# Optimization experiments

Hardware: AMD Instinct MI355X
Metric: run time of the kernel (lower is better)

## Reference

```python
import jax, jax.numpy as jnp
import numpy as np

GROUP_SIZE = 128

def _dequantize(qweight, wscales, wzeros):
    # qweight: [N, K//2] packed bytes, two uint4 values per byte
    # low nibble = even k index, high nibble = odd k index
    N, Kh = qweight.shape
    K = Kh * 2
    low = qweight & 0xF
    high = (qweight >> 4) & 0xF
    w_int = jnp.stack([low, high], axis=-1).reshape(N, K).astype(jnp.float32)  # [N, K]
    G = K // GROUP_SIZE  # number of groups along K
    w_grp = w_int.reshape(N, G, GROUP_SIZE)
    s = wscales.T.reshape(N, G, 1)   # wscales: [G, N] -> [N, G, 1]
    z = wzeros.T.reshape(N, G, 1)
    return ((w_grp - z) * s).reshape(N, K)  # [N, K] dequantized

def setup_inputs() -> dict:
    key = jax.random.key(0)
    k1, k2, k3, k4, k5 = jax.random.split(key, 5)
    M, K, N = 4096, 4096, 12288
    G = K // GROUP_SIZE
    x = jax.random.normal(k1, (M, K), dtype=jnp.float32)
    qweight = jax.random.randint(k2, (N, K // 2), 0, 256, dtype=jnp.int32)
    wscales = jax.random.uniform(k3, (G, N), dtype=jnp.float32) * 0.05
    wzeros = jax.random.uniform(k4, (G, N), dtype=jnp.float32) * 15.0
    bias = jax.random.normal(k5, (N,), dtype=jnp.float32)
    return {"x": x, "qweight": qweight, "wscales": wscales, "wzeros": wzeros, "bias": bias}

def reference(x, qweight, wscales, wzeros, bias):
    # AWQ W4A16 linear: y = x @ dequant(W)^T + b
    w = _dequantize(qweight, wscales, wzeros)  # [N, K]
    return jnp.einsum('mk,nk->mn', x, w) + bias
```

## Files before the change

kernel.cpp:

```cpp
#include <hip/hip_runtime.h>

#define M_DIM 4096
#define K_DIM 4096
#define N_DIM 12288
#define BM 256
#define BN 256
#define BK 64
#define NT (K_DIM / BK)

typedef __bf16 bf16x8  __attribute__((ext_vector_type(8)));
typedef float  floatx16 __attribute__((ext_vector_type(16)));

__global__ __launch_bounds__(256) void xcast_kernel(const float* __restrict__ x,
                                                    __bf16* __restrict__ xb) {
    int idx = blockIdx.x * 256 + threadIdx.x;
    const float4* xv = (const float4*)x;
    float4 a = xv[idx * 2];
    float4 b = xv[idx * 2 + 1];
    bf16x8 o;
    o[0] = (__bf16)a.x; o[1] = (__bf16)a.y; o[2] = (__bf16)a.z; o[3] = (__bf16)a.w;
    o[4] = (__bf16)b.x; o[5] = (__bf16)b.y; o[6] = (__bf16)b.z; o[7] = (__bf16)b.w;
    ((bf16x8*)xb)[idx] = o;
}

__global__ __launch_bounds__(256) void dequant_kernel(const int* __restrict__ qw,
                                                      const float* __restrict__ scales,
                                                      const float* __restrict__ zeros,
                                                      __bf16* __restrict__ wb) {
    int idx = blockIdx.x * 256 + threadIdx.x;
    int n  = idx >> 9;
    int jq = (idx & 511) << 2;
    int g  = jq >> 6;
    float s = scales[g * N_DIM + n];
    float z = zeros[g * N_DIM + n];
    int4 q = *(const int4*)(qw + (size_t)n * (K_DIM / 2) + jq);
    bf16x8 o;
    o[0] = (__bf16)(((float)(q.x & 15)        - z) * s);
    o[1] = (__bf16)(((float)((q.x >> 4) & 15) - z) * s);
    o[2] = (__bf16)(((float)(q.y & 15)        - z) * s);
    o[3] = (__bf16)(((float)((q.y >> 4) & 15) - z) * s);
    o[4] = (__bf16)(((float)(q.z & 15)        - z) * s);
    o[5] = (__bf16)(((float)((q.z >> 4) & 15) - z) * s);
    o[6] = (__bf16)(((float)(q.w & 15)        - z) * s);
    o[7] = (__bf16)(((float)((q.w >> 4) & 15) - z) * s);
    *(bf16x8*)(wb + (size_t)n * K_DIM + (size_t)jq * 2) = o;
}

__global__ __launch_bounds__(512, 2) void gemm_kernel(const __bf16* __restrict__ A,
                                                      const __bf16* __restrict__ B,
                                                      const float* __restrict__ bias,
                                                      float* __restrict__ C) {
    __shared__ __bf16 As[2 * 2 * 256 * 32];
    __shared__ __bf16 Bs[2 * 2 * 256 * 32];

    const int tid  = threadIdx.x;
    const int wave = tid >> 6;
    const int lane = tid & 63;
    const int l32  = lane & 31;
    const int half = lane >> 5;
    const int side = wave >> 2;
    const int aw   = wave & 3;
    const int wm   = side * 128;
    const int wn   = aw * 64;
    const int bm0  = blockIdx.x * BM;
    const int bn0  = blockIdx.y * BN;

    const int r16  = lane >> 2;
    const int sl4  = lane & 3;
    const int bswz = ((lane >> 3) & 3) ^ ((lane >> 5) & 3);
    const int key0 = sl4 ^ bswz;
    const int key1 = key0 ^ 2;
    const __bf16* sA0 = A + (size_t)(bm0 + 32 * wave +      r16) * K_DIM + key0 * 8;
    const __bf16* sA1 = A + (size_t)(bm0 + 32 * wave + 16 + r16) * K_DIM + key1 * 8;
    const __bf16* sB0 = B + (size_t)(bn0 + 32 * wave +      r16) * K_DIM + key0 * 8;
    const __bf16* sB1 = B + (size_t)(bn0 + 32 * wave + 16 + r16) * K_DIM + key1 * 8;
    const int dst0 = wave * 1024;
    const int dst1 = wave * 1024 + 512;

    #define GLOAD(G, L) __builtin_amdgcn_global_load_lds( \
        (const __attribute__((address_space(1))) void*)(G), \
        (__attribute__((address_space(3))) void*)(L), 16, 0, 0)

    const int swzr = ((l32 >> 1) ^ (l32 >> 3)) & 3;
    const int koE  = ((half)     ^ swzr) << 3;
    const int koO  = ((2 | half) ^ swzr) << 3;
    const int rA0 = (wm +  0 + l32) * 32;
    const int rA1 = (wm + 32 + l32) * 32;
    const int rA2 = (wm + 64 + l32) * 32;
    const int rA3 = (wm + 96 + l32) * 32;
    const int rB0 = (wn +  0 + l32) * 32;
    const int rB1 = (wn + 32 + l32) * 32;

    #define MF(AF, BF, ACC) __builtin_amdgcn_mfma_f32_32x32x16_bf16((AF), (BF), (ACC), 0, 0, 0)

    floatx16 acc00 = {}, acc01 = {}, acc10 = {}, acc11 = {};
    floatx16 acc20 = {}, acc21 = {}, acc30 = {}, acc31 = {};

    GLOAD(sA0,      As + dst0);        GLOAD(sA1,      As + dst1);
    GLOAD(sB0,      Bs + dst0);        GLOAD(sB1,      Bs + dst1);
    GLOAD(sA0 + 32, As + 8192 + dst0); GLOAD(sA1 + 32, As + 8192 + dst1);
    GLOAD(sB0 + 32, Bs + 8192 + dst0); GLOAD(sB1 + 32, Bs + 8192 + dst1);
    asm volatile("s_waitcnt vmcnt(4)" ::: "memory");
    __builtin_amdgcn_s_barrier();

    #define READS(HOFF, KO) \
        a0 = *(const bf16x8*)(As + curo + (HOFF) + rA0 + (KO)); \
        b0 = *(const bf16x8*)(Bs + curo + (HOFF) + rB0 + (KO)); \
        a1 = *(const bf16x8*)(As + curo + (HOFF) + rA1 + (KO)); \
        b1 = *(const bf16x8*)(Bs + curo + (HOFF) + rB1 + (KO)); \
        a2 = *(const bf16x8*)(As + curo + (HOFF) + rA2 + (KO)); \
        a3 = *(const bf16x8*)(As + curo + (HOFF) + rA3 + (KO));

    #define MFMAS \
        __builtin_amdgcn_s_setprio(1); \
        acc00 = MF(a0, b0, acc00); acc10 = MF(a1, b0, acc10); \
        acc01 = MF(a0, b1, acc01); acc11 = MF(a1, b1, acc11); \
        acc20 = MF(a2, b0, acc20); acc21 = MF(a2, b1, acc21); \
        acc30 = MF(a3, b0, acc30); acc31 = MF(a3, b1, acc31); \
        __builtin_amdgcn_s_setprio(0);

    for (int kt = 0; kt < NT; ++kt) {
        const int curo = (kt & 1) * 16384;
        const int nxto = 16384 - curo;
        const int k0n  = ((kt + 1) & (NT - 1)) * BK;
        bf16x8 a0, a1, a2, a3, b0, b1;

        READS(0, koE);
        __builtin_amdgcn_s_barrier();
        MFMAS;
        __builtin_amdgcn_s_barrier();

        READS(0, koO);
        GLOAD(sA0 + k0n, As + nxto + dst0); GLOAD(sA1 + k0n, As + nxto + dst1);
        GLOAD(sB0 + k0n, Bs + nxto + dst0); GLOAD(sB1 + k0n, Bs + nxto + dst1);
        asm volatile("s_waitcnt vmcnt(4)" ::: "memory");
        __builtin_amdgcn_s_barrier();
        MFMAS;
        __builtin_amdgcn_s_barrier();

        READS(8192, koE);
        __builtin_amdgcn_s_barrier();
        MFMAS;
        __builtin_amdgcn_s_barrier();

        READS(8192, koO);
        GLOAD(sA0 + k0n + 32, As + nxto + 8192 + dst0);
        GLOAD(sA1 + k0n + 32, As + nxto + 8192 + dst1);
        GLOAD(sB0 + k0n + 32, Bs + nxto + 8192 + dst0);
        GLOAD(sB1 + k0n + 32, Bs + nxto + 8192 + dst1);
        asm volatile("s_waitcnt vmcnt(4)" ::: "memory");
        __builtin_amdgcn_s_barrier();
        MFMAS;
        __builtin_amdgcn_s_barrier();
    }

    #define EPI(ACC, MI, NI) { \
        const int col = bn0 + wn + (NI) * 32 + l32; \
        const float bv = bias[col]; \
        _Pragma("unroll") \
        for (int r = 0; r < 16; ++r) { \
            const int row = bm0 + wm + (MI) * 32 + half * 4 + (r & 3) + 8 * (r >> 2); \
            C[(size_t)row * N_DIM + col] = ACC[r] + bv; \
        } }
    EPI(acc00, 0, 0); EPI(acc01, 0, 1);
    EPI(acc10, 1, 0); EPI(acc11, 1, 1);
    EPI(acc20, 2, 0); EPI(acc21, 2, 1);
    EPI(acc30, 3, 0); EPI(acc31, 3, 1);
}

extern "C" void kernel_launch(void* const* d_in, const int* in_sizes, int n_in,
                              void* d_out, int out_size, void* d_ws, size_t ws_size,
                              hipStream_t stream) {
    const float* x      = (const float*)d_in[0];
    const int*   qw     = (const int*)d_in[1];
    const float* scales = (const float*)d_in[2];
    const float* zeros  = (const float*)d_in[3];
    const float* bias   = (const float*)d_in[4];
    float* out = (float*)d_out;

    __bf16* xb = (__bf16*)d_ws;
    __bf16* wb = (__bf16*)((char*)d_ws + (size_t)M_DIM * K_DIM * 2);

    xcast_kernel<<<(M_DIM * K_DIM / 8) / 256, 256, 0, stream>>>(x, xb);
    dequant_kernel<<<(N_DIM * (K_DIM / 2) / 4) / 256, 256, 0, stream>>>(qw, scales, zeros, wb);

    dim3 grid(M_DIM / BM, N_DIM / BN);
    gemm_kernel<<<grid, 512, 0, stream>>>(xb, wb, bias, out);
}
```

Before: 729.1 us.

## Deepen GEMM LDS pipeline to three in-flight stages and swizzle block order

Restructures the GEMM main loop so each phase reads both even and odd k-fragments from one 32-wide LDS slab, issues the global-to-LDS load for a slab three stages ahead, and then runs 16 MFMAs between just two barriers. This keeps more global loads in flight and halves the barrier count per k-step. It also remaps block indices so groups of consecutive blocks share N tiles, aiming for better L2 reuse. The cost is higher register pressure from 12 live fragments and a tighter ring of LDS slots that depends on the vmcnt(8) wait being correct.

New measurement: 727.1 us. About the same (-0.3%).

```diff
diff --git a/kernel.cpp b/kernel.cpp
--- a/kernel.cpp
+++ b/kernel.cpp
@@ -7,6 +7,8 @@
 #define BN 256
 #define BK 64
 #define NT (K_DIM / BK)
+#define HALF 8192
+#define BUF  16384
 
 typedef __bf16 bf16x8  __attribute__((ext_vector_type(8)));
 typedef float  floatx16 __attribute__((ext_vector_type(16)));
@@ -50,8 +52,8 @@
                                                       const __bf16* __restrict__ B,
                                                       const float* __restrict__ bias,
                                                       float* __restrict__ C) {
-    __shared__ __bf16 As[2 * 2 * 256 * 32];
-    __shared__ __bf16 Bs[2 * 2 * 256 * 32];
+    __shared__ __bf16 As[2 * BUF];
+    __shared__ __bf16 Bs[2 * BUF];
 
     const int tid  = threadIdx.x;
     const int wave = tid >> 6;
@@ -62,8 +64,11 @@
     const int aw   = wave & 3;
     const int wm   = side * 128;
     const int wn   = aw * 64;
-    const int bm0  = blockIdx.x * BM;
-    const int bn0  = blockIdx.y * BN;
+
+    const int bid = blockIdx.y * 16 + blockIdx.x;
+    const int sw  = (bid & 7) * 96 + (bid >> 3);
+    const int bm0 = (sw & 15) * BM;
+    const int bn0 = (sw >> 4) * BN;
 
     const int r16  = lane >> 2;
     const int sl4  = lane & 3;
@@ -81,6 +86,10 @@
         (const __attribute__((address_space(1))) void*)(G), \
         (__attribute__((address_space(3))) void*)(L), 16, 0, 0)
 
+    #define STAGE(CS, HO) \
+        GLOAD(sA0 + (CS), As + (HO) + dst0); GLOAD(sA1 + (CS), As + (HO) + dst1); \
+        GLOAD(sB0 + (CS), Bs + (HO) + dst0); GLOAD(sB1 + (CS), Bs + (HO) + dst1);
+
     const int swzr = ((l32 >> 1) ^ (l32 >> 3)) & 3;
     const int koE  = ((half)     ^ swzr) << 3;
     const int koO  = ((2 | half) ^ swzr) << 3;
@@ -96,62 +105,46 @@
     floatx16 acc00 = {}, acc01 = {}, acc10 = {}, acc11 = {};
     floatx16 acc20 = {}, acc21 = {}, acc30 = {}, acc31 = {};
 
-    GLOAD(sA0,      As + dst0);        GLOAD(sA1,      As + dst1);
-    GLOAD(sB0,      Bs + dst0);        GLOAD(sB1,      Bs + dst1);
-    GLOAD(sA0 + 32, As + 8192 + dst0); GLOAD(sA1 + 32, As + 8192 + dst1);
-    GLOAD(sB0 + 32, Bs + 8192 + dst0); GLOAD(sB1 + 32, Bs + 8192 + dst1);
-    asm volatile("s_waitcnt vmcnt(4)" ::: "memory");
+    #define PHASE(HO, CS, SHO) { \
+        bf16x8 a0e = *(const bf16x8*)(As + (HO) + rA0 + koE); \
+        bf16x8 a1e = *(const bf16x8*)(As + (HO) + rA1 + koE); \
+        bf16x8 a2e = *(const bf16x8*)(As + (HO) + rA2 + koE); \
+        bf16x8 a3e = *(const bf16x8*)(As + (HO) + rA3 + koE); \
+        bf16x8 b0e = *(const bf16x8*)(Bs + (HO) + rB0 + koE); \
+        bf16x8 b1e = *(const bf16x8*)(Bs + (HO) + rB1 + koE); \
+        bf16x8 a0o = *(const bf16x8*)(As + (HO) + rA0 + koO); \
+        bf16x8 a1o = *(const bf16x8*)(As + (HO) + rA1 + koO); \
+        bf16x8 a2o = *(const bf16x8*)(As + (HO) + rA2 + koO); \
+        bf16x8 a3o = *(const bf16x8*)(As + (HO) + rA3 + koO); \
+        bf16x8 b0o = *(const bf16x8*)(Bs + (HO) + rB0 + koO); \
+        bf16x8 b1o = *(const bf16x8*)(Bs + (HO) + rB1 + koO); \
+        STAGE(CS, SHO); \
+        asm volatile("s_waitcnt vmcnt(8)" ::: "memory"); \
+        __builtin_amdgcn_s_barrier(); \
+        __builtin_amdgcn_s_setprio(1); \
+        acc00 = MF(a0e, b0e, acc00); acc10 = MF(a1e, b0e, acc10); \
+        acc01 = MF(a0e, b1e, acc01); acc11 = MF(a1e, b1e, acc11); \
+        acc20 = MF(a2e, b0e, acc20); acc21 = MF(a2e, b1e, acc21); \
+        acc30 = MF(a3e, b0e, acc30); acc31 = MF(a3e, b1e, acc31); \
+        acc00 = MF(a0o, b0o, acc00); acc10 = MF(a1o, b0o, acc10); \
+        acc01 = MF(a0o, b1o, acc01); acc11 = MF(a1o, b1o, acc11); \
+        acc20 = MF(a2o, b0o, acc20); acc21 = MF(a2o, b1o, acc21); \
+        acc30 = MF(a3o, b0o, acc30); acc31 = MF(a3o, b1o, acc31); \
+        __builtin_amdgcn_s_setprio(0); \
+        __builtin_amdgcn_s_barrier(); }
+
+    STAGE(0,  0);
+    STAGE(32, HALF);
+    STAGE(64, BUF);
+    asm volatile("s_waitcnt vmcnt(8)" ::: "memory");
     __builtin_amdgcn_s_barrier();
 
-    #define READS(HOFF, KO) \
-        a0 = *(const bf16x8*)(As + curo + (HOFF) + rA0 + (KO)); \
-        b0 = *(const bf16x8*)(Bs + curo + (HOFF) + rB0 + (KO)); \
-        a1 = *(const bf16x8*)(As + curo + (HOFF) + rA1 + (KO)); \
-        b1 = *(const bf16x8*)(Bs + curo + (HOFF) + rB1 + (KO)); \
-        a2 = *(const bf16x8*)(As + curo + (HOFF) + rA2 + (KO)); \
-        a3 = *(const bf16x8*)(As + curo + (HOFF) + rA3 + (KO));
-
-    #define MFMAS \
-        __builtin_amdgcn_s_setprio(1); \
-        acc00 = MF(a0, b0, acc00); acc10 = MF(a1, b0, acc10); \
-        acc01 = MF(a0, b1, acc01); acc11 = MF(a1, b1, acc11); \
-        acc20 = MF(a2, b0, acc20); acc21 = MF(a2, b1, acc21); \
-        acc30 = MF(a3, b0, acc30); acc31 = MF(a3, b1, acc31); \
-        __builtin_amdgcn_s_setprio(0);
-
-    for (int kt = 0; kt < NT; ++kt) {
-        const int curo = (kt & 1) * 16384;
-        const int nxto = 16384 - curo;
-        const int k0n  = ((kt + 1) & (NT - 1)) * BK;
-        bf16x8 a0, a1, a2, a3, b0, b1;
-
-        READS(0, koE);
-        __builtin_amdgcn_s_barrier();
-        MFMAS;
-        __builtin_amdgcn_s_barrier();
-
-        READS(0, koO);
-        GLOAD(sA0 + k0n, As + nxto + dst0); GLOAD(sA1 + k0n, As + nxto + dst1);
-        GLOAD(sB0 + k0n, Bs + nxto + dst0); GLOAD(sB1 + k0n, Bs + nxto + dst1);
-        asm volatile("s_waitcnt vmcnt(4)" ::: "memory");
-        __builtin_amdgcn_s_barrier();
-        MFMAS;
-        __builtin_amdgcn_s_barrier();
-
-        READS(8192, koE);
-        __builtin_amdgcn_s_barrier();
-        MFMAS;
-        __builtin_amdgcn_s_barrier();
-
-        READS(8192, koO);
-        GLOAD(sA0 + k0n + 32, As + nxto + 8192 + dst0);
-        GLOAD(sA1 + k0n + 32, As + nxto + 8192 + dst1);
-        GLOAD(sB0 + k0n + 32, Bs + nxto + 8192 + dst0);
-        GLOAD(sB1 + k0n + 32, Bs + nxto + 8192 + dst1);
-        asm volatile("s_waitcnt vmcnt(4)" ::: "memory");
-        __builtin_amdgcn_s_barrier();
-        MFMAS;
-        __builtin_amdgcn_s_barrier();
+    for (int it = 0; it < NT / 2; ++it) {
+        const int k64 = it * 128;
+        PHASE(0,    (k64 +  96) & 4095, BUF + HALF);
+        PHASE(HALF, (k64 + 128) & 4095, 0);
+        PHASE(BUF,        (k64 + 160) & 4095, HALF);
+        PHASE(BUF + HALF, (k64 + 192) & 4095, BUF);
     }
 
     #define EPI(ACC, MI, NI) { \
```
